# Kernel tuning notes

Hardware: AMD Instinct MI355X
Metric: run time of the kernel (lower is better)

## Reference

```python
import jax, jax.numpy as jnp
import numpy as np

N_ROBOTS = 2048   # N
EMBED = 256       # d (= global_embed_dim)
M_GROUPS = 4096   # M
GROUP_K = 16      # fixed group size K
N_OBS = 64


def setup_inputs() -> dict:
    key = jax.random.key(0)
    ks = jax.random.split(key, 6)
    h = jax.random.normal(ks[0], (N_ROBOTS, EMBED), dtype=jnp.float32)
    attn_rr = jax.random.uniform(ks[1], (N_ROBOTS, N_ROBOTS), dtype=jnp.float32)
    attn_ro = jax.random.uniform(ks[2], (N_ROBOTS, N_OBS), dtype=jnp.float32)
    dist_to_goal = jax.random.uniform(ks[3], (N_ROBOTS,), dtype=jnp.float32)
    clearance = jax.random.uniform(ks[4], (N_ROBOTS,), dtype=jnp.float32)
    groups = jax.random.randint(ks[5], (M_GROUPS, GROUP_K), 0, N_ROBOTS)
    return {"h": h, "attn_rr": attn_rr, "attn_ro": attn_ro,
            "dist_to_goal": dist_to_goal, "clearance": clearance, "groups": groups}


def reference(h, attn_rr, attn_ro, dist_to_goal, clearance, groups):
    n_robots, d = h.shape
    m, k = groups.shape
    dt = h.dtype

    # global embedding = mean of per-robot embeddings (h_glob=None path)
    h_glob = h.mean(axis=0)                                   # (d,)

    # pooled group embedding, mean pooling
    h_g = h[groups].mean(axis=1)                              # (M, d)

    # normalized group size
    size_feat = jnp.full((m, 1), k / 3.0, dtype=dt)

    # A_in: mean attention among distinct-index pairs within group
    sub = attn_rr[groups[:, :, None], groups[:, None, :]]     # (M, K, K)
    neq = (groups[:, :, None] != groups[:, None, :]).astype(dt)
    cnt_in = neq.sum(axis=(1, 2))
    a_in = (sub * neq).sum(axis=(1, 2)) / jnp.maximum(cnt_in, 1.0)

    # unique membership indicator per group (set semantics, like torch's group_set)
    member = jnp.zeros((m, n_robots), dtype=dt).at[
        jnp.arange(m)[:, None], groups].set(1.0)              # (M, N)
    n_out = n_robots - member.sum(axis=1)                     # |outside set|

    # A_out: mean attention from group rows (with multiplicity K) to outside columns
    rows = attn_rr[groups]                                    # (M, K, N)
    out_sum = rows.sum(axis=(1, 2)) - jnp.einsum('mkn,mn->m', rows, member)
    a_out = out_sum / jnp.maximum(k * n_out, 1.0)

    # A_obs: mean attention from group robots to all obstacles
    a_obs = attn_ro[groups].mean(axis=(1, 2))

    attn_stats = jnp.stack([a_in, a_out, a_obs], axis=1)      # (M, 3)

    # extra per-robot feature aggregations: dist_to_goal->mean, clearance->min
    ex_dist = dist_to_goal[groups].mean(axis=1, keepdims=True)
    ex_clr = clearance[groups].min(axis=1, keepdims=True)

    h_glob_b = jnp.broadcast_to(h_glob[None, :], (m, d))
    return jnp.concatenate([h_g, h_glob_b, size_feat, attn_stats, ex_dist, ex_clr], axis=1)
```

## Files before the change

kernel.cpp:

```cpp
#include <hip/hip_runtime.h>
#include <hip/hip_bf16.h>

#define N_ROBOTS 2048
#define EMBED 256
#define M_GROUPS 4096
#define GROUP_K 16
#define N_OBS 64
#define OUT_W 518


__global__ __launch_bounds__(256) void precompute_kernel(
    const float* __restrict__ h,
    const float* __restrict__ attn_rr,
    const float* __restrict__ attn_ro,
    float* __restrict__ ws)
{
    const int b = blockIdx.x;
    const int t = threadIdx.x;

    if (b < N_ROBOTS) {
        const float4* row4 = (const float4*)(attn_rr + (size_t)b * N_ROBOTS);
        const float4 a = row4[t];
        const float4 c = row4[t + 256];
        float s = (a.x + a.y) + (a.z + a.w) + (c.x + c.y) + (c.z + c.w);

        float so = (t < N_OBS) ? attn_ro[b * N_OBS + t] : 0.f;

        #pragma unroll
        for (int off = 32; off > 0; off >>= 1) {
            s  += __shfl_down(s,  off);
            so += __shfl_down(so, off);
        }
        __shared__ float lds[8];
        const int wave = t >> 6, lane = t & 63;
        if (lane == 0) { lds[wave] = s; lds[4 + wave] = so; }
        __syncthreads();
        if (t == 0) {
            ws[b]            = lds[0] + lds[1] + lds[2] + lds[3];
            ws[N_ROBOTS + b] = lds[4] + lds[5] + lds[6] + lds[7];
        }
    } else {
        const int bb   = b - N_ROBOTS;
        const int col  = bb * 32 + (t & 31);
        const int chnk = t >> 5;
        float s = 0.f;
        const int r0 = chnk * (N_ROBOTS / 8);
        for (int r = r0; r < r0 + N_ROBOTS / 8; ++r)
            s += h[(size_t)r * EMBED + col];
        __shared__ float hg[8][32];
        hg[chnk][t & 31] = s;
        __syncthreads();
        if (t < 32) {
            float tot = 0.f;
            #pragma unroll
            for (int c = 0; c < 8; ++c) tot += hg[c][t];
            ws[2 * N_ROBOTS + bb * 32 + t] = tot;
        }
    }
}

__global__ __launch_bounds__(64) void group_kernel(
    const float* __restrict__ h,
    const float* __restrict__ attn_rr,
    const float* __restrict__ dist,
    const float* __restrict__ clr,
    const int*   __restrict__ groups,
    const float* __restrict__ ws,
    float* __restrict__ out)
{
    const int m    = blockIdx.x;
    const int lane = threadIdx.x;

    __shared__ int   gl[GROUP_K];
    __shared__ float uql[GROUP_K];

    if (lane < GROUP_K) gl[lane] = groups[m * GROUP_K + lane];
    __syncthreads();

    if (lane < GROUP_K) {
        const int gt = gl[lane];
        float u = 1.f;
        for (int p = 0; p < lane; ++p) if (gl[p] == gt) { u = 0.f; break; }
        uql[lane] = u;
    }
    __syncthreads();

    float2 ha = {0.f, 0.f}, hb = {0.f, 0.f};
    #pragma unroll
    for (int k = 0; k < GROUP_K; ++k) {
        const float2* hr = (const float2*)(h + (size_t)gl[k] * EMBED);
        const float2 x = hr[lane];
        const float2 y = hr[lane + 64];
        ha.x += x.x; ha.y += x.y;
        hb.x += y.x; hb.y += y.y;
    }

    const int   j  = lane & 15;
    const int   gj = gl[j];
    const float uj = uql[j];
    float s_in = 0.f, s_cnt = 0.f, s_uq = 0.f;
    #pragma unroll
    for (int q = 0; q < 4; ++q) {
        const int gi = gl[(lane >> 4) + 4 * q];
        const float v = attn_rr[(size_t)gi * N_ROBOTS + gj];
        if (gi != gj) { s_in += v; s_cnt += 1.f; }
        s_uq += uj * v;
    }

    float m_rr = 0.f, m_ro = 0.f, m_ds = 0.f, m_cl = 1e30f, m_uq = 0.f;
    if (lane < GROUP_K) {
        const int gt = gl[lane];
        m_rr = ws[gt];
        m_ro = ws[N_ROBOTS + gt];
        m_ds = dist[gt];
        m_cl = clr[gt];
        m_uq = uql[lane];
    }
    #pragma unroll
    for (int off = 8; off > 0; off >>= 1) {
        m_rr += __shfl_down(m_rr, off);
        m_ro += __shfl_down(m_ro, off);
        m_ds += __shfl_down(m_ds, off);
        m_cl  = fminf(m_cl, __shfl_down(m_cl, off));
        m_uq += __shfl_down(m_uq, off);
    }
    #pragma unroll
    for (int off = 32; off > 0; off >>= 1) {
        s_in  += __shfl_down(s_in,  off);
        s_cnt += __shfl_down(s_cnt, off);
        s_uq  += __shfl_down(s_uq,  off);
    }

    const size_t base = (size_t)m * OUT_W;
    float2* out2 = (float2*)(out + base);
    const float2* wg2 = (const float2*)(ws + 2 * N_ROBOTS);

    float2 r;
    r.x = ha.x * (1.f / GROUP_K); r.y = ha.y * (1.f / GROUP_K);
    out2[lane] = r;
    r.x = hb.x * (1.f / GROUP_K); r.y = hb.y * (1.f / GROUP_K);
    out2[lane + 64] = r;
    float2 g0 = wg2[lane], g1 = wg2[lane + 64];
    g0.x *= (1.f / N_ROBOTS); g0.y *= (1.f / N_ROBOTS);
    g1.x *= (1.f / N_ROBOTS); g1.y *= (1.f / N_ROBOTS);
    out2[lane + 128] = g0;
    out2[lane + 192] = g1;

    if (lane == 0) {
        const float a_in  = s_in / fmaxf(s_cnt, 1.f);
        const float n_out = (float)N_ROBOTS - m_uq;
        const float a_out = (m_rr - s_uq) / fmaxf((float)GROUP_K * n_out, 1.f);
        const float a_obs = m_ro * (1.f / (GROUP_K * N_OBS));
        out[base + 512] = (float)GROUP_K / 3.0f;
        out[base + 513] = a_in;
        out[base + 514] = a_out;
        out[base + 515] = a_obs;
        out[base + 516] = m_ds * (1.f / GROUP_K);
        out[base + 517] = m_cl;
    }
}

extern "C" void kernel_launch(void* const* d_in, const int* in_sizes, int n_in,
                              void* d_out, int out_size, void* d_ws, size_t ws_size,
                              hipStream_t stream) {
    const float* h       = (const float*)d_in[0];
    const float* attn_rr = (const float*)d_in[1];
    const float* attn_ro = (const float*)d_in[2];
    const float* dist    = (const float*)d_in[3];
    const float* clr     = (const float*)d_in[4];
    const int*   groups  = (const int*)d_in[5];
    float* out = (float*)d_out;
    float* ws  = (float*)d_ws;

    precompute_kernel<<<N_ROBOTS + 8, 256, 0, stream>>>(h, attn_rr, attn_ro, ws);
    group_kernel<<<M_GROUPS, 64, 0, stream>>>(h, attn_rr, dist, clr, groups, ws, out);
}
```

Baseline: 36.81 us.

## Fuse precompute and group kernels into one persistent kernel with grid barrier

Merges the row-sum precompute and the per-group kernel into a single 512-block kernel separated by a software grid barrier built on atomics in the workspace. Each wave first reduces one attn_rr row and then handles two groups, so the per-block work is coarser. This removes one kernel launch and the gap between the two launches, but adds a memset, a spin-wait barrier that needs all 512 blocks resident at once, and fewer blocks for hiding latency in the gather phase.

Measured after the change: 65.67 us. +78.4%, slower.

```diff
diff --git a/kernel.cpp b/kernel.cpp
--- a/kernel.cpp
+++ b/kernel.cpp
@@ -1,5 +1,4 @@
 #include <hip/hip_runtime.h>
-#include <hip/hip_bf16.h>
 
 #define N_ROBOTS 2048
 #define EMBED 256
@@ -7,156 +6,184 @@
 #define GROUP_K 16
 #define N_OBS 64
 #define OUT_W 518
-
-
-__global__ __launch_bounds__(256) void precompute_kernel(
+#define NBLOCKS 512
+
+
+__device__ inline void grid_barrier(unsigned int* bar, int t) {
+    __syncthreads();
+    if (t == 0) {
+        const unsigned int e0 = __atomic_load_n(&bar[1], __ATOMIC_RELAXED);
+        __threadfence();
+        const unsigned int pos = __atomic_fetch_add(&bar[0], 1u, __ATOMIC_RELAXED) + 1u;
+        if (pos == NBLOCKS) {
+            __threadfence();
+            __atomic_fetch_add(&bar[1], 1u, __ATOMIC_RELEASE);
+        } else {
+            for (int it = 0; it < (1 << 24); ++it) {
+                if (__atomic_load_n(&bar[1], __ATOMIC_RELAXED) != e0) break;
+                __builtin_amdgcn_s_sleep(2);
+            }
+        }
+        __threadfence();
+    }
+    __syncthreads();
+}
+
+__global__ __launch_bounds__(256, 2) void fused_kernel(
     const float* __restrict__ h,
     const float* __restrict__ attn_rr,
     const float* __restrict__ attn_ro,
-    float* __restrict__ ws)
+    const float* __restrict__ dist,
+    const float* __restrict__ clr,
+    const int*   __restrict__ groups,
+    float* __restrict__ ws,
+    float* __restrict__ out)
 {
-    const int b = blockIdx.x;
-    const int t = threadIdx.x;
-
-    if (b < N_ROBOTS) {
-        const float4* row4 = (const float4*)(attn_rr + (size_t)b * N_ROBOTS);
-        const float4 a = row4[t];
-        const float4 c = row4[t + 256];
-        float s = (a.x + a.y) + (a.z + a.w) + (c.x + c.y) + (c.z + c.w);
-
-        float so = (t < N_OBS) ? attn_ro[b * N_OBS + t] : 0.f;
+    const int bid  = blockIdx.x;
+    const int t    = threadIdx.x;
+    const int w    = t >> 6;
+    const int lane = t & 63;
+
+    __shared__ float hg[8][32];
+    __shared__ int   gl[4][2][GROUP_K];
+    __shared__ float uql[4][2][GROUP_K];
+
+    {
+        const int r = 4 * bid + w;
+        const float4* row4 = (const float4*)(attn_rr + (size_t)r * N_ROBOTS);
+        float s = 0.f;
+        #pragma unroll
+        for (int i = 0; i < 8; ++i) {
+            const float4 a = row4[i * 64 + lane];
+            s += (a.x + a.y) + (a.z + a.w);
+        }
+        float so = attn_ro[(size_t)r * N_OBS + lane];
 
         #pragma unroll
         for (int off = 32; off > 0; off >>= 1) {
             s  += __shfl_down(s,  off);
             so += __shfl_down(so, off);
         }
-        __shared__ float lds[8];
-        const int wave = t >> 6, lane = t & 63;
-        if (lane == 0) { lds[wave] = s; lds[4 + wave] = so; }
-        __syncthreads();
-        if (t == 0) {
-            ws[b]            = lds[0] + lds[1] + lds[2] + lds[3];
-            ws[N_ROBOTS + b] = lds[4] + lds[5] + lds[6] + lds[7];
-        }
-    } else {
-        const int bb   = b - N_ROBOTS;
-        const int col  = bb * 32 + (t & 31);
-        const int chnk = t >> 5;
-        float s = 0.f;
-        const int r0 = chnk * (N_ROBOTS / 8);
-        for (int r = r0; r < r0 + N_ROBOTS / 8; ++r)
-            s += h[(size_t)r * EMBED + col];
-        __shared__ float hg[8][32];
-        hg[chnk][t & 31] = s;
-        __syncthreads();
-        if (t < 32) {
-            float tot = 0.f;
-            #pragma unroll
-            for (int c = 0; c < 8; ++c) tot += hg[c][t];
-            ws[2 * N_ROBOTS + bb * 32 + t] = tot;
-        }
-    }
-}
-
-__global__ __launch_bounds__(64) void group_kernel(
-    const float* __restrict__ h,
-    const float* __restrict__ attn_rr,
-    const float* __restrict__ dist,
-    const float* __restrict__ clr,
-    const int*   __restrict__ groups,
-    const float* __restrict__ ws,
-    float* __restrict__ out)
-{
-    const int m    = blockIdx.x;
-    const int lane = threadIdx.x;
-
-    __shared__ int   gl[GROUP_K];
-    __shared__ float uql[GROUP_K];
-
-    if (lane < GROUP_K) gl[lane] = groups[m * GROUP_K + lane];
-    __syncthreads();
-
-    if (lane < GROUP_K) {
-        const int gt = gl[lane];
+        if (lane == 0) { ws[r] = s; ws[N_ROBOTS + r] = so; }
+
+        if (bid < 8) {
+            const int col  = bid * 32 + (t & 31);
+            const int chnk = t >> 5;
+            float s2 = 0.f;
+            const int r0 = chnk * 256;
+            for (int r2 = r0; r2 < r0 + 256; ++r2)
+                s2 += h[(size_t)r2 * EMBED + col];
+            hg[chnk][t & 31] = s2;
+            __syncthreads();
+            if (t < 32) {
+                float tot = 0.f;
+                #pragma unroll
+                for (int c = 0; c < 8; ++c) tot += hg[c][t];
+                ws[2 * N_ROBOTS + bid * 32 + t] = tot;
+            }
+        }
+    }
+
+    grid_barrier((unsigned int*)(ws + 2 * N_ROBOTS + EMBED), t);
+
+    const int m0 = 8 * bid + 2 * w;
+
+    if (lane < 2 * GROUP_K) {
+        const int g2 = lane >> 4, idx = lane & 15;
+        gl[w][g2][idx] = groups[(size_t)(m0 + g2) * GROUP_K + idx];
+    }
+    __syncthreads();
+    if (lane < 2 * GROUP_K) {
+        const int g2 = lane >> 4, idx = lane & 15;
+        const int gt = gl[w][g2][idx];
         float u = 1.f;
-        for (int p = 0; p < lane; ++p) if (gl[p] == gt) { u = 0.f; break; }
-        uql[lane] = u;
-    }
-    __syncthreads();
-
-    float2 ha = {0.f, 0.f}, hb = {0.f, 0.f};
+        for (int p = 0; p < idx; ++p) if (gl[w][g2][p] == gt) { u = 0.f; break; }
+        uql[w][g2][idx] = u;
+    }
+    __syncthreads();
+
+    float2 ha[2], hb[2];
+    float  s_in[2], s_cnt[2], s_uq[2];
+    float  m_rr[2], m_ro[2], m_ds[2], m_cl[2], m_uq[2];
+
     #pragma unroll
-    for (int k = 0; k < GROUP_K; ++k) {
-        const float2* hr = (const float2*)(h + (size_t)gl[k] * EMBED);
-        const float2 x = hr[lane];
-        const float2 y = hr[lane + 64];
-        ha.x += x.x; ha.y += x.y;
-        hb.x += y.x; hb.y += y.y;
-    }
-
-    const int   j  = lane & 15;
-    const int   gj = gl[j];
-    const float uj = uql[j];
-    float s_in = 0.f, s_cnt = 0.f, s_uq = 0.f;
+    for (int g2 = 0; g2 < 2; ++g2) {
+        ha[g2] = make_float2(0.f, 0.f); hb[g2] = make_float2(0.f, 0.f);
+        #pragma unroll
+        for (int k = 0; k < GROUP_K; ++k) {
+            const float2* hr = (const float2*)(h + (size_t)gl[w][g2][k] * EMBED);
+            const float2 x = hr[lane];
+            const float2 y = hr[lane + 64];
+            ha[g2].x += x.x; ha[g2].y += x.y;
+            hb[g2].x += y.x; hb[g2].y += y.y;
+        }
+
+        const int   j  = lane & 15;
+        const int   gj = gl[w][g2][j];
+        const float uj = uql[w][g2][j];
+        s_in[g2] = 0.f; s_cnt[g2] = 0.f; s_uq[g2] = 0.f;
+        #pragma unroll
+        for (int q = 0; q < 4; ++q) {
+            const int gi = gl[w][g2][(lane >> 4) + 4 * q];
+            const float v = attn_rr[(size_t)gi * N_ROBOTS + gj];
+            if (gi != gj) { s_in[g2] += v; s_cnt[g2] += 1.f; }
+            s_uq[g2] += uj * v;
+        }
+
+        m_rr[g2] = 0.f; m_ro[g2] = 0.f; m_ds[g2] = 0.f; m_cl[g2] = 1e30f; m_uq[g2] = 0.f;
+        if (lane < GROUP_K) {
+            const int gt = gl[w][g2][lane];
+            m_rr[g2] = ws[gt];
+            m_ro[g2] = ws[N_ROBOTS + gt];
+            m_ds[g2] = dist[gt];
+            m_cl[g2] = clr[gt];
+            m_uq[g2] = uql[w][g2][lane];
+        }
+        #pragma unroll
+        for (int off = 8; off > 0; off >>= 1) {
+            m_rr[g2] += __shfl_down(m_rr[g2], off);
+            m_ro[g2] += __shfl_down(m_ro[g2], off);
+            m_ds[g2] += __shfl_down(m_ds[g2], off);
+            m_cl[g2]  = fminf(m_cl[g2], __shfl_down(m_cl[g2], off));
+            m_uq[g2] += __shfl_down(m_uq[g2], off);
+        }
+        #pragma unroll
+        for (int off = 32; off > 0; off >>= 1) {
+            s_in[g2]  += __shfl_down(s_in[g2],  off);
+            s_cnt[g2] += __shfl_down(s_cnt[g2], off);
+            s_uq[g2]  += __shfl_down(s_uq[g2],  off);
+        }
+    }
+
+    const float2* wg2 = (const float2*)(ws + 2 * N_ROBOTS);
+    const float2 g0 = wg2[lane], g1 = wg2[lane + 64];
+
     #pragma unroll
-    for (int q = 0; q < 4; ++q) {
-        const int gi = gl[(lane >> 4) + 4 * q];
-        const float v = attn_rr[(size_t)gi * N_ROBOTS + gj];
-        if (gi != gj) { s_in += v; s_cnt += 1.f; }
-        s_uq += uj * v;
-    }
-
-    float m_rr = 0.f, m_ro = 0.f, m_ds = 0.f, m_cl = 1e30f, m_uq = 0.f;
-    if (lane < GROUP_K) {
-        const int gt = gl[lane];
-        m_rr = ws[gt];
-        m_ro = ws[N_ROBOTS + gt];
-        m_ds = dist[gt];
-        m_cl = clr[gt];
-        m_uq = uql[lane];
-    }
-    #pragma unroll
-    for (int off = 8; off > 0; off >>= 1) {
-        m_rr += __shfl_down(m_rr, off);
-        m_ro += __shfl_down(m_ro, off);
-        m_ds += __shfl_down(m_ds, off);
-        m_cl  = fminf(m_cl, __shfl_down(m_cl, off));
-        m_uq += __shfl_down(m_uq, off);
-    }
-    #pragma unroll
-    for (int off = 32; off > 0; off >>= 1) {
-        s_in  += __shfl_down(s_in,  off);
-        s_cnt += __shfl_down(s_cnt, off);
-        s_uq  += __shfl_down(s_uq,  off);
-    }
-
-    const size_t base = (size_t)m * OUT_W;
-    float2* out2 = (float2*)(out + base);
-    const float2* wg2 = (const float2*)(ws + 2 * N_ROBOTS);
-
-    float2 r;
-    r.x = ha.x * (1.f / GROUP_K); r.y = ha.y * (1.f / GROUP_K);
-    out2[lane] = r;
-    r.x = hb.x * (1.f / GROUP_K); r.y = hb.y * (1.f / GROUP_K);
-    out2[lane + 64] = r;
-    float2 g0 = wg2[lane], g1 = wg2[lane + 64];
-    g0.x *= (1.f / N_ROBOTS); g0.y *= (1.f / N_ROBOTS);
-    g1.x *= (1.f / N_ROBOTS); g1.y *= (1.f / N_ROBOTS);
-    out2[lane + 128] = g0;
-    out2[lane + 192] = g1;
-
-    if (lane == 0) {
-        const float a_in  = s_in / fmaxf(s_cnt, 1.f);
-        const float n_out = (float)N_ROBOTS - m_uq;
-        const float a_out = (m_rr - s_uq) / fmaxf((float)GROUP_K * n_out, 1.f);
-        const float a_obs = m_ro * (1.f / (GROUP_K * N_OBS));
-        out[base + 512] = (float)GROUP_K / 3.0f;
-        out[base + 513] = a_in;
-        out[base + 514] = a_out;
-        out[base + 515] = a_obs;
-        out[base + 516] = m_ds * (1.f / GROUP_K);
-        out[base + 517] = m_cl;
+    for (int g2 = 0; g2 < 2; ++g2) {
+        const size_t base = (size_t)(m0 + g2) * OUT_W;
+        float2* out2 = (float2*)(out + base);
+        float2 r2;
+        r2.x = ha[g2].x * (1.f / GROUP_K); r2.y = ha[g2].y * (1.f / GROUP_K);
+        out2[lane] = r2;
+        r2.x = hb[g2].x * (1.f / GROUP_K); r2.y = hb[g2].y * (1.f / GROUP_K);
+        out2[lane + 64] = r2;
+        r2.x = g0.x * (1.f / N_ROBOTS); r2.y = g0.y * (1.f / N_ROBOTS);
+        out2[lane + 128] = r2;
+        r2.x = g1.x * (1.f / N_ROBOTS); r2.y = g1.y * (1.f / N_ROBOTS);
+        out2[lane + 192] = r2;
+
+        if (lane == 0) {
+            const float a_in  = s_in[g2] / fmaxf(s_cnt[g2], 1.f);
+            const float n_out = (float)N_ROBOTS - m_uq[g2];
+            const float a_out = (m_rr[g2] - s_uq[g2]) / fmaxf((float)GROUP_K * n_out, 1.f);
+            const float a_obs = m_ro[g2] * (1.f / (GROUP_K * N_OBS));
+            out[base + 512] = (float)GROUP_K / 3.0f;
+            out[base + 513] = a_in;
+            out[base + 514] = a_out;
+            out[base + 515] = a_obs;
+            out[base + 516] = m_ds[g2] * (1.f / GROUP_K);
+            out[base + 517] = m_cl[g2];
+        }
     }
 }
 
@@ -172,6 +199,8 @@
     float* out = (float*)d_out;
     float* ws  = (float*)d_ws;
 
-    precompute_kernel<<<N_ROBOTS + 8, 256, 0, stream>>>(h, attn_rr, attn_ro, ws);
-    group_kernel<<<M_GROUPS, 64, 0, stream>>>(h, attn_rr, dist, clr, groups, ws, out);
+    hipMemsetAsync(ws + 2 * N_ROBOTS + EMBED, 0, 2 * sizeof(unsigned int), stream);
+
+    fused_kernel<<<NBLOCKS, 256, 0, stream>>>(h, attn_rr, attn_ro, dist, clr,
+                                              groups, ws, out);
 }
```

## Invert attention gather into per-row buckets served from LDS

Applied to the files above, without the earlier changes.

Adds a prep kernel that buckets group ids by member robot using atomic cursors and precomputes per-group uniqueness masks and distinct-pair counts. The row kernel, which already streams each attn_rr row to get its row sum, now stages the row in LDS and serves every group's in-group gathers from it. It accumulates the masked sums with float atomics. This replaces the scattered random reads of attn_rr in the old group kernel. The cost is an extra memset and kernel launch, atomic contention, nondeterministic summation order, and groups silently dropped if a robot appears in more than CAP groups.

After: 45.96 us. +24.8%, slower.

```diff
diff --git a/kernel.cpp b/kernel.cpp
--- a/kernel.cpp
+++ b/kernel.cpp
@@ -1,5 +1,4 @@
 #include <hip/hip_runtime.h>
-#include <hip/hip_bf16.h>
 
 #define N_ROBOTS 2048
 #define EMBED 256
@@ -7,61 +6,137 @@
 #define GROUP_K 16
 #define N_OBS 64
 #define OUT_W 518
-
-
-__global__ __launch_bounds__(256) void precompute_kernel(
+#define CAP 128
+
+#define WS_RR    0
+#define WS_RO    2048
+#define WS_HG    4096
+#define WS_CUR   4352
+#define WS_NEQ   6400
+#define WS_UQ    10496
+#define WS_META  14592
+#define WS_BUCK  22784
+
+__global__ __launch_bounds__(256) void prep_kernel(
     const float* __restrict__ h,
-    const float* __restrict__ attn_rr,
-    const float* __restrict__ attn_ro,
+    const int*   __restrict__ groups,
     float* __restrict__ ws)
 {
-    const int b = blockIdx.x;
-    const int t = threadIdx.x;
-
-    if (b < N_ROBOTS) {
-        const float4* row4 = (const float4*)(attn_rr + (size_t)b * N_ROBOTS);
-        const float4 a = row4[t];
-        const float4 c = row4[t + 256];
-        float s = (a.x + a.y) + (a.z + a.w) + (c.x + c.y) + (c.z + c.w);
-
-        float so = (t < N_OBS) ? attn_ro[b * N_OBS + t] : 0.f;
-
-        #pragma unroll
-        for (int off = 32; off > 0; off >>= 1) {
-            s  += __shfl_down(s,  off);
-            so += __shfl_down(so, off);
-        }
-        __shared__ float lds[8];
-        const int wave = t >> 6, lane = t & 63;
-        if (lane == 0) { lds[wave] = s; lds[4 + wave] = so; }
-        __syncthreads();
-        if (t == 0) {
-            ws[b]            = lds[0] + lds[1] + lds[2] + lds[3];
-            ws[N_ROBOTS + b] = lds[4] + lds[5] + lds[6] + lds[7];
-        }
-    } else {
-        const int bb   = b - N_ROBOTS;
-        const int col  = bb * 32 + (t & 31);
+    const int bid = blockIdx.x, t = threadIdx.x;
+
+    if (bid < 8) {
+        __shared__ float hg[8][32];
+        const int col  = bid * 32 + (t & 31);
         const int chnk = t >> 5;
-        float s = 0.f;
-        const int r0 = chnk * (N_ROBOTS / 8);
-        for (int r = r0; r < r0 + N_ROBOTS / 8; ++r)
-            s += h[(size_t)r * EMBED + col];
-        __shared__ float hg[8][32];
-        hg[chnk][t & 31] = s;
+        float s2 = 0.f;
+        const int r0 = chnk * 256;
+        for (int r = r0; r < r0 + 256; ++r)
+            s2 += h[(size_t)r * EMBED + col];
+        hg[chnk][t & 31] = s2;
         __syncthreads();
         if (t < 32) {
             float tot = 0.f;
             #pragma unroll
             for (int c = 0; c < 8; ++c) tot += hg[c][t];
-            ws[2 * N_ROBOTS + bb * 32 + t] = tot;
-        }
-    }
-}
-
-__global__ __launch_bounds__(64) void group_kernel(
+            ws[WS_HG + bid * 32 + t] = tot;
+        }
+        return;
+    }
+
+    const int tid = (bid - 8) * 256 + t;
+    unsigned* cursor = (unsigned*)(ws + WS_CUR);
+    int*      bucket = (int*)(ws + WS_BUCK);
+
+    #pragma unroll
+    for (int i = 0; i < 4; ++i) {
+        const int e = tid + i * 16384;
+        const int r = groups[e];
+        const unsigned pos = atomicAdd(&cursor[r], 1u);
+        if (pos < CAP) bucket[r * CAP + pos] = e >> 4;
+    }
+
+    if (tid < M_GROUPS) {
+        const int m = tid;
+        int g[GROUP_K];
+        #pragma unroll
+        for (int k = 0; k < GROUP_K; ++k) g[k] = groups[m * GROUP_K + k];
+        unsigned mask = 0; int ucnt = 0, ceq = 0;
+        #pragma unroll
+        for (int i = 0; i < GROUP_K; ++i) {
+            bool u = true;
+            for (int p = 0; p < i; ++p) if (g[p] == g[i]) { u = false; break; }
+            if (u) { mask |= 1u << i; ++ucnt; }
+            for (int jj = 0; jj < GROUP_K; ++jj) ceq += (g[i] == g[jj]);
+        }
+        uint2 v;
+        v.x = mask | ((unsigned)ucnt << 16);
+        v.y = (unsigned)(GROUP_K * GROUP_K - ceq);
+        ((uint2*)(ws + WS_META))[m] = v;
+    }
+}
+
+__global__ __launch_bounds__(256) void row_kernel(
+    const float* __restrict__ attn_rr,
+    const float* __restrict__ attn_ro,
+    const int*   __restrict__ groups,
+    float* __restrict__ ws)
+{
+    const int r = blockIdx.x;
+    const int t = threadIdx.x;
+
+    __shared__ float row[N_ROBOTS];
+    __shared__ float red[8];
+
+    const float4* row4 = (const float4*)(attn_rr + (size_t)r * N_ROBOTS);
+    const float4 a = row4[t];
+    const float4 b = row4[t + 256];
+    ((float4*)row)[t]       = a;
+    ((float4*)row)[t + 256] = b;
+    float s  = (a.x + a.y) + (a.z + a.w) + (b.x + b.y) + (b.z + b.w);
+    float so = (t < N_OBS) ? attn_ro[(size_t)r * N_OBS + t] : 0.f;
+
+    #pragma unroll
+    for (int off = 32; off > 0; off >>= 1) {
+        s  += __shfl_down(s,  off);
+        so += __shfl_down(so, off);
+    }
+    const int w = t >> 6, lane = t & 63;
+    if (lane == 0) { red[w] = s; red[4 + w] = so; }
+    __syncthreads();
+    if (t == 0) {
+        ws[WS_RR + r] = red[0] + red[1] + red[2] + red[3];
+        ws[WS_RO + r] = red[4];
+    }
+
+    const unsigned cnt = ((const unsigned*)(ws + WS_CUR))[r];
+    const unsigned occ = cnt < CAP ? cnt : CAP;
+    const int* bucket = (const int*)(ws + WS_BUCK) + r * CAP;
+    const uint2* meta = (const uint2*)(ws + WS_META);
+    float* acc_neq = ws + WS_NEQ;
+    float* acc_uq  = ws + WS_UQ;
+
+    const int sg = t >> 4, l = t & 15;
+    for (unsigned o = sg; o < occ; o += 16) {
+        const int m  = bucket[o];
+        const int gj = groups[m * GROUP_K + l];
+        const unsigned mask = meta[m].x;
+        const float v  = row[gj];
+        float s0 = (gj != r)          ? v : 0.f;
+        float s1 = ((mask >> l) & 1u) ? v : 0.f;
+        #pragma unroll
+        for (int off = 8; off > 0; off >>= 1) {
+            s0 += __shfl_down(s0, off);
+            s1 += __shfl_down(s1, off);
+        }
+        if (l == 0) {
+            atomicAdd(&acc_neq[m], s0);
+            atomicAdd(&acc_uq[m],  s1);
+        }
+    }
+}
+
+__global__ __launch_bounds__(64) void finalize_kernel(
     const float* __restrict__ h,
-    const float* __restrict__ attn_rr,
     const float* __restrict__ dist,
     const float* __restrict__ clr,
     const int*   __restrict__ groups,
@@ -71,18 +146,8 @@
     const int m    = blockIdx.x;
     const int lane = threadIdx.x;
 
-    __shared__ int   gl[GROUP_K];
-    __shared__ float uql[GROUP_K];
-
+    __shared__ int gl[GROUP_K];
     if (lane < GROUP_K) gl[lane] = groups[m * GROUP_K + lane];
-    __syncthreads();
-
-    if (lane < GROUP_K) {
-        const int gt = gl[lane];
-        float u = 1.f;
-        for (int p = 0; p < lane; ++p) if (gl[p] == gt) { u = 0.f; break; }
-        uql[lane] = u;
-    }
     __syncthreads();
 
     float2 ha = {0.f, 0.f}, hb = {0.f, 0.f};
@@ -95,26 +160,13 @@
         hb.x += y.x; hb.y += y.y;
     }
 
-    const int   j  = lane & 15;
-    const int   gj = gl[j];
-    const float uj = uql[j];
-    float s_in = 0.f, s_cnt = 0.f, s_uq = 0.f;
-    #pragma unroll
-    for (int q = 0; q < 4; ++q) {
-        const int gi = gl[(lane >> 4) + 4 * q];
-        const float v = attn_rr[(size_t)gi * N_ROBOTS + gj];
-        if (gi != gj) { s_in += v; s_cnt += 1.f; }
-        s_uq += uj * v;
-    }
-
-    float m_rr = 0.f, m_ro = 0.f, m_ds = 0.f, m_cl = 1e30f, m_uq = 0.f;
+    float m_rr = 0.f, m_ro = 0.f, m_ds = 0.f, m_cl = 1e30f;
     if (lane < GROUP_K) {
         const int gt = gl[lane];
-        m_rr = ws[gt];
-        m_ro = ws[N_ROBOTS + gt];
+        m_rr = ws[WS_RR + gt];
+        m_ro = ws[WS_RO + gt];
         m_ds = dist[gt];
         m_cl = clr[gt];
-        m_uq = uql[lane];
     }
     #pragma unroll
     for (int off = 8; off > 0; off >>= 1) {
@@ -122,24 +174,23 @@
         m_ro += __shfl_down(m_ro, off);
         m_ds += __shfl_down(m_ds, off);
         m_cl  = fminf(m_cl, __shfl_down(m_cl, off));
-        m_uq += __shfl_down(m_uq, off);
-    }
-    #pragma unroll
-    for (int off = 32; off > 0; off >>= 1) {
-        s_in  += __shfl_down(s_in,  off);
-        s_cnt += __shfl_down(s_cnt, off);
-        s_uq  += __shfl_down(s_uq,  off);
-    }
+    }
+
+    const uint2 mt = ((const uint2*)(ws + WS_META))[m];
+    const int   ucnt  = (int)(mt.x >> 16);
+    const float c_neq = (float)mt.y;
+    const float s_neq = ws[WS_NEQ + m];
+    const float s_uq  = ws[WS_UQ + m];
 
     const size_t base = (size_t)m * OUT_W;
     float2* out2 = (float2*)(out + base);
-    const float2* wg2 = (const float2*)(ws + 2 * N_ROBOTS);
-
-    float2 r;
-    r.x = ha.x * (1.f / GROUP_K); r.y = ha.y * (1.f / GROUP_K);
-    out2[lane] = r;
-    r.x = hb.x * (1.f / GROUP_K); r.y = hb.y * (1.f / GROUP_K);
-    out2[lane + 64] = r;
+    const float2* wg2 = (const float2*)(ws + WS_HG);
+
+    float2 r2;
+    r2.x = ha.x * (1.f / GROUP_K); r2.y = ha.y * (1.f / GROUP_K);
+    out2[lane] = r2;
+    r2.x = hb.x * (1.f / GROUP_K); r2.y = hb.y * (1.f / GROUP_K);
+    out2[lane + 64] = r2;
     float2 g0 = wg2[lane], g1 = wg2[lane + 64];
     g0.x *= (1.f / N_ROBOTS); g0.y *= (1.f / N_ROBOTS);
     g1.x *= (1.f / N_ROBOTS); g1.y *= (1.f / N_ROBOTS);
@@ -147,8 +198,8 @@
     out2[lane + 192] = g1;
 
     if (lane == 0) {
-        const float a_in  = s_in / fmaxf(s_cnt, 1.f);
-        const float n_out = (float)N_ROBOTS - m_uq;
+        const float a_in  = s_neq / fmaxf(c_neq, 1.f);
+        const float n_out = (float)(N_ROBOTS - ucnt);
         const float a_out = (m_rr - s_uq) / fmaxf((float)GROUP_K * n_out, 1.f);
         const float a_obs = m_ro * (1.f / (GROUP_K * N_OBS));
         out[base + 512] = (float)GROUP_K / 3.0f;
@@ -172,6 +223,9 @@
     float* out = (float*)d_out;
     float* ws  = (float*)d_ws;
 
-    precompute_kernel<<<N_ROBOTS + 8, 256, 0, stream>>>(h, attn_rr, attn_ro, ws);
-    group_kernel<<<M_GROUPS, 64, 0, stream>>>(h, attn_rr, dist, clr, groups, ws, out);
-}
+    hipMemsetAsync(ws + WS_CUR, 0, (WS_META - WS_CUR) * sizeof(float), stream);
+
+    prep_kernel<<<8 + 64, 256, 0, stream>>>(h, groups, ws);
+    row_kernel<<<N_ROBOTS, 256, 0, stream>>>(attn_rr, attn_ro, groups, ws);
+    finalize_kernel<<<M_GROUPS, 64, 0, stream>>>(h, dist, clr, groups, ws, out);
+}
```
